# Optimization experiments

Hardware: AMD Instinct MI355X
Metric: run time of the kernel (lower is better)

## Reference

```python
import jax, jax.numpy as jnp
import numpy as np

B, NS, NF, D, H = 64, 16, 4096, 128, 256  # batch, n_slots, n_feat, slot_dim, mlp_hidden
EPS_LN = 1e-5
EPS_ATT = 1e-8


def _layernorm(x, g, b):
    mu = x.mean(-1, keepdims=True)
    var = x.var(-1, keepdims=True)
    return (x - mu) / jnp.sqrt(var + EPS_LN) * g + b


def setup_inputs() -> dict:
    key = jax.random.key(0)
    ks = jax.random.split(key, 8)
    s = 0.02  # init scale for weights
    return {
        "t": jnp.zeros((), jnp.float32),
        "slots": jax.random.normal(ks[0], (B, NS, D), jnp.float32),
        "k": jax.random.normal(ks[1], (B, NF, D), jnp.float32),
        "v": jax.random.normal(ks[2], (B, NF, D), jnp.float32),
        "Wq": jax.random.normal(ks[3], (D, D), jnp.float32) * s,           # eqx Linear weight [out,in], no bias
        "ln_slots_g": jnp.ones((D,), jnp.float32),
        "ln_slots_b": jnp.zeros((D,), jnp.float32),
        "W_ih": jax.random.normal(ks[4], (3 * D, D), jnp.float32) * s,     # GRUCell input weights
        "W_hh": jax.random.normal(ks[5], (3 * D, D), jnp.float32) * s,     # GRUCell hidden weights
        "b_ih": jnp.zeros((3 * D,), jnp.float32),
        "b_n": jnp.zeros((D,), jnp.float32),
        "ln_ff_g": jnp.ones((D,), jnp.float32),
        "ln_ff_b": jnp.zeros((D,), jnp.float32),
        "W0": jax.random.normal(ks[6], (H, D), jnp.float32) * s,
        "b0": jnp.zeros((H,), jnp.float32),
        "W1": jax.random.normal(ks[7], (D, H), jnp.float32) * s,
        "b1": jnp.zeros((D,), jnp.float32),
    }


def reference(t, slots, k, v, Wq, ln_slots_g, ln_slots_b,
              W_ih, W_hh, b_ih, b_n, ln_ff_g, ln_ff_b, W0, b0, W1, b1):
    scale = D ** (-0.5)
    # LayerNorm over slot features, then query projection
    slots_norm = _layernorm(slots, ln_slots_g, ln_slots_b)
    q = jnp.einsum('bnd,ed->bne', slots_norm, Wq)                    # [B,NS,D]
    # Doubly-normalized slot attention: softmax over slots (axis=1), renorm over features
    att_logits = jnp.einsum('bnd,bmd->bnm', q, k) * scale            # [B,NS,NF]
    att = jax.nn.softmax(att_logits, axis=1)
    att = att / (att.sum(axis=-1, keepdims=True) + EPS_ATT)
    attended = jnp.einsum('bnm,bmd->bnd', att, v)                    # [B,NS,D]
    # GRUCell (equinox semantics): gates order (reset, input, new)
    igates = jnp.einsum('bnd,ed->bne', attended, W_ih) + b_ih        # [B,NS,3D]
    hgates = jnp.einsum('bnd,ed->bne', slots, W_hh)                  # [B,NS,3D]
    ir, ii, inew = jnp.split(igates, 3, axis=-1)
    hr, hi, hnew = jnp.split(hgates, 3, axis=-1)
    reset = jax.nn.sigmoid(ir + hr)
    inp = jax.nn.sigmoid(ii + hi)
    new = jnp.tanh(inew + reset * (hnew + b_n))
    gru_out = new + inp * (slots - new)                              # [B,NS,D]
    # LayerNorm -> MLP residual
    gru_normed = _layernorm(gru_out, ln_ff_g, ln_ff_b)
    h = jax.nn.relu(jnp.einsum('bnd,hd->bnh', gru_normed, W0) + b0)
    h = jnp.einsum('bnh,dh->bnd', h, W1) + b1
    target = gru_out + h
    return target - slots
```

## Files before the change

### kernel.cpp

```cpp
#include <hip/hip_runtime.h>
#include <hip/hip_bf16.h>
#include <math.h>

#define B_  64
#define NS_ 16
#define NF_ 4096
#define D_  128
#define H_  256


typedef __attribute__((ext_vector_type(8))) short bf16x8;
typedef __attribute__((ext_vector_type(4))) float f32x4;

__device__ __forceinline__ bf16x8 as_bf16x8(uint4 u) {
    union { uint4 u; bf16x8 h; } c; c.u = u; return c.h;
}

__device__ __forceinline__ unsigned int pk_bf16(float a, float b) {
    unsigned int ua = __float_as_uint(a), ub = __float_as_uint(b);
    ua = (ua + 0x7FFFu + ((ua >> 16) & 1u)) >> 16;
    ub = (ub + 0x7FFFu + ((ub >> 16) & 1u)) >> 16;
    return ua | (ub << 16);
}

__device__ __forceinline__ float dot4(float4 a, float4 b) {
    return a.x * b.x + a.y * b.y + a.z * b.z + a.w * b.w;
}

__global__ __launch_bounds__(128) void k_q(
    const float* __restrict__ slots, const float* __restrict__ Wq,
    const float* __restrict__ lng, const float* __restrict__ lnb,
    unsigned int* __restrict__ q_out, float* __restrict__ acc, float* __restrict__ den) {
    const int b = blockIdx.x;
    const int t = threadIdx.x;
    __shared__ float sl_s[16][128];
    __shared__ float norm_s[16][128];
    __shared__ float st_s[16][8][2];
    __shared__ float mu_s[16], rs_s[16];
    __shared__ float q_s[16][128];

    const float4* sp = (const float4*)(slots + (size_t)b * 2048);
#pragma unroll
    for (int i = 0; i < 4; ++i) {
        int f = i * 128 + t;
        *(float4*)&sl_s[f >> 5][(f & 31) * 4] = sp[f];
    }
    __syncthreads();

    {
        int n = t >> 3, j = t & 7;
        float s1 = 0.f, s2 = 0.f;
#pragma unroll
        for (int d2 = 0; d2 < 16; ++d2) {
            float x = sl_s[n][j * 16 + d2];
            s1 += x; s2 += x * x;
        }
        st_s[n][j][0] = s1; st_s[n][j][1] = s2;
    }
    __syncthreads();
    if (t < 16) {
        float s1 = 0.f, s2 = 0.f;
#pragma unroll
        for (int j = 0; j < 8; ++j) { s1 += st_s[t][j][0]; s2 += st_s[t][j][1]; }
        float mu = s1 * (1.0f / 128.0f);
        float var = s2 * (1.0f / 128.0f) - mu * mu;
        mu_s[t] = mu;
        rs_s[t] = rsqrtf(var + 1e-5f);
    }
    __syncthreads();

    float gl = lng[t], bl = lnb[t];
#pragma unroll
    for (int n = 0; n < 16; ++n)
        norm_s[n][t] = (sl_s[n][t] - mu_s[n]) * rs_s[n] * gl + bl;
    __syncthreads();

    const float4* wq = (const float4*)(Wq + (size_t)t * 128);
    float qn[16];
#pragma unroll
    for (int n = 0; n < 16; ++n) qn[n] = 0.f;
#pragma unroll 4
    for (int j = 0; j < 32; ++j) {
        float4 w4 = wq[j];
#pragma unroll
        for (int n = 0; n < 16; ++n) qn[n] += dot4(w4, *(const float4*)&norm_s[n][4 * j]);
    }
#pragma unroll
    for (int n = 0; n < 16; ++n) q_s[n][t] = qn[n];

    float4 z4 = make_float4(0.f, 0.f, 0.f, 0.f);
    float4* ab = (float4*)(acc + (size_t)b * 2048);
#pragma unroll
    for (int i = 0; i < 4; ++i) ab[i * 128 + t] = z4;
    if (t < 16) den[b * 16 + t] = 0.f;
    __syncthreads();

    unsigned int* qo = q_out + (size_t)b * 1024;
#pragma unroll
    for (int i = 0; i < 8; ++i) {
        int u = i * 128 + t;
        int n = u >> 6, e2 = u & 63;
        qo[n * 64 + e2] = pk_bf16(q_s[n][2 * e2], q_s[n][2 * e2 + 1]);
    }
}

template<int PART>
__global__ __launch_bounds__(256) void k_attn(
    const float* __restrict__ kg_, const float* __restrict__ vg_,
    const unsigned int* __restrict__ q_u, float* __restrict__ acc_g,
    float* __restrict__ part, float* __restrict__ denom_g) {
    const int t = threadIdx.x;
    const int w = t >> 6, l = t & 63;
    const int b = blockIdx.y;
    const int lm = l & 15;
    const int g  = l >> 4;
    const int dcol = t & 127;
    const int nh = t >> 7;

    __shared__ unsigned int lds_u[5632];
    unsigned int* k_s = lds_u;
    float*        p_s = (float*)(lds_u + 4352);

    uint4 qA[4];
    {
        const uint4* qb = (const uint4*)q_u + ((b * 16 + lm) * 16);
#pragma unroll
        for (int kk = 0; kk < 4; ++kk) qA[kk] = qb[kk * 4 + g];
    }

    float acc[16];
#pragma unroll
    for (int i = 0; i < 16; ++i) acc[i] = 0.f;
    float dn[4] = {0.f, 0.f, 0.f, 0.f};

    const size_t mbase = (size_t)b * NF_ + blockIdx.x * 256;
    const float4* kg4 = (const float4*)kg_ + (mbase + w * 16) * 32;
    const float*  vgp = vg_ + mbase * 128 + dcol;

    for (int sub = 0; sub < 4; ++sub) {
        const float* vt = vgp + (size_t)(sub * 64 + nh * 32) * 128;

        const float4* kp = kg4 + sub * 64 * 32;
        float4 ka[4], kb4[4];
#pragma unroll
        for (int i = 0; i < 4; ++i) ka[i] = kp[i * 64 + l];
#pragma unroll
        for (int i = 0; i < 4; ++i) kb4[i] = kp[(4 + i) * 64 + l];

        float vva[8], vvb[8];
#pragma unroll
        for (int i = 0; i < 8; ++i) vva[i] = vt[i * 128];
#pragma unroll
        for (int i = 0; i < 8; ++i) vvb[i] = vt[(8 + i) * 128];

#pragma unroll
        for (int i = 0; i < 4; ++i) {
            int r = w * 16 + 2 * i + (l >> 5);
            *(uint2*)&k_s[r * 68 + 2 * (l & 31)] =
                make_uint2(pk_bf16(ka[i].x, ka[i].y), pk_bf16(ka[i].z, ka[i].w));
        }
#pragma unroll
        for (int i = 0; i < 4; ++i) {
            int r = w * 16 + 2 * (4 + i) + (l >> 5);
            *(uint2*)&k_s[r * 68 + 2 * (l & 31)] =
                make_uint2(pk_bf16(kb4[i].x, kb4[i].y), pk_bf16(kb4[i].z, kb4[i].w));
        }

        f32x4 sacc = {0.f, 0.f, 0.f, 0.f};
#pragma unroll
        for (int kk = 0; kk < 4; ++kk) {
            uint4 kf = *(const uint4*)&k_s[(w * 16 + lm) * 68 + kk * 16 + g * 4];
            sacc = __builtin_amdgcn_mfma_f32_16x16x32_bf16(
                as_bf16x8(qA[kk]), as_bf16x8(kf), sacc, 0, 0, 0);
        }
        const float scale = 0.08838834764831845f;
        float e0 = __expf(sacc[0] * scale);
        float e1 = __expf(sacc[1] * scale);
        float e2 = __expf(sacc[2] * scale);
        float e3 = __expf(sacc[3] * scale);
        float se = (e0 + e1) + (e2 + e3);
        se += __shfl_xor(se, 16);
        se += __shfl_xor(se, 32);
        float rse = __builtin_amdgcn_rcpf(se);
        float4 pv4 = make_float4(e0 * rse, e1 * rse, e2 * rse, e3 * rse);
        dn[0] += pv4.x; dn[1] += pv4.y; dn[2] += pv4.z; dn[3] += pv4.w;
        *(float4*)&p_s[(w * 16 + lm) * 20 + g * 4] = pv4;
        __syncthreads();

#define PV_CONSUME(VREG, BASE)                                              \
        {                                                                   \
            _Pragma("unroll")                                               \
            for (int i = 0; i < 8; ++i) {                                   \
                int m = nh * 32 + (BASE) + i;                               \
                float vvi = VREG[i];                                        \
                float4 pa = *(const float4*)&p_s[m * 20 + 0];               \
                float4 pb = *(const float4*)&p_s[m * 20 + 4];               \
                float4 pc = *(const float4*)&p_s[m * 20 + 8];               \
                float4 pd = *(const float4*)&p_s[m * 20 + 12];              \
                acc[0]  = fmaf(pa.x, vvi, acc[0]);                          \
                acc[1]  = fmaf(pa.y, vvi, acc[1]);                          \
                acc[2]  = fmaf(pa.z, vvi, acc[2]);                          \
                acc[3]  = fmaf(pa.w, vvi, acc[3]);                          \
                acc[4]  = fmaf(pb.x, vvi, acc[4]);                          \
                acc[5]  = fmaf(pb.y, vvi, acc[5]);                          \
                acc[6]  = fmaf(pb.z, vvi, acc[6]);                          \
                acc[7]  = fmaf(pb.w, vvi, acc[7]);                          \
                acc[8]  = fmaf(pc.x, vvi, acc[8]);                          \
                acc[9]  = fmaf(pc.y, vvi, acc[9]);                          \
                acc[10] = fmaf(pc.z, vvi, acc[10]);                         \
                acc[11] = fmaf(pc.w, vvi, acc[11]);                         \
                acc[12] = fmaf(pd.x, vvi, acc[12]);                         \
                acc[13] = fmaf(pd.y, vvi, acc[13]);                         \
                acc[14] = fmaf(pd.z, vvi, acc[14]);                         \
                acc[15] = fmaf(pd.w, vvi, acc[15]);                         \
            }                                                               \
        }
        PV_CONSUME(vva, 0)
#pragma unroll
        for (int i = 0; i < 8; ++i) vva[i] = vt[(16 + i) * 128];
        PV_CONSUME(vvb, 8)
#pragma unroll
        for (int i = 0; i < 8; ++i) vvb[i] = vt[(24 + i) * 128];
        PV_CONSUME(vva, 16)
        PV_CONSUME(vvb, 24)
#undef PV_CONSUME
        __syncthreads();
    }

#pragma unroll
    for (int m = 1; m <= 8; m <<= 1) {
#pragma unroll
        for (int r = 0; r < 4; ++r) dn[r] += __shfl_xor(dn[r], m);
    }
    if (lm == 0) {
#pragma unroll
        for (int r = 0; r < 4; ++r)
            atomicAdd(denom_g + b * 16 + g * 4 + r, dn[r]);
    }
    float* red = (float*)lds_u;
    if (nh == 1) {
#pragma unroll
        for (int n = 0; n < 16; ++n) red[dcol * 17 + n] = acc[n];
    }
    __syncthreads();
    if (nh == 0) {
        if (PART) {
            float* base = part + ((size_t)(b * 16 + blockIdx.x) * 16) * 128 + dcol;
#pragma unroll
            for (int n = 0; n < 16; ++n)
                base[n * 128] = acc[n] + red[dcol * 17 + n];
        } else {
            float* base = acc_g + (size_t)b * 2048 + dcol;
#pragma unroll
            for (int n = 0; n < 16; ++n)
                atomicAdd(base + n * 128, acc[n] + red[dcol * 17 + n]);
        }
    }
}

template<int PART>
__global__ __launch_bounds__(256) void k_final(
    const float* __restrict__ acc_g, const float* __restrict__ part,
    const float* __restrict__ denom_g, const float* __restrict__ slots,
    const float* __restrict__ W_ih, const float* __restrict__ W_hh,
    const float* __restrict__ b_ih, const float* __restrict__ b_n,
    const float* __restrict__ ffg, const float* __restrict__ ffb,
    const float* __restrict__ W0, const float* __restrict__ b0,
    const float* __restrict__ W1, const float* __restrict__ b1,
    float* __restrict__ out) {
    const int bn0 = blockIdx.x * 4;
    const int t = threadIdx.x;
    __shared__ float att_s[4][128], slot_s[4][128];
    __shared__ float gates_s[4][4][128];
    __shared__ float gru_s[4][128], gn_s[4][128];
    __shared__ float h_s[4][256];

#pragma unroll
    for (int idx = t; idx < 512; idx += 256) {
        int bi = idx >> 7, d = idx & 127;
        int bn = bn0 + bi;
        float den = denom_g[bn] + 1e-8f;
        float s;
        if (PART) {
            const float* pp = part + ((size_t)(bn >> 4) * 256 + (bn & 15)) * 128 + d;
            s = 0.f;
#pragma unroll
            for (int c = 0; c < 16; ++c) s += pp[c * 2048];
        } else {
            s = acc_g[(size_t)bn * 128 + d];
        }
        att_s[bi][d] = s / den;
        slot_s[bi][d] = slots[(size_t)bn * 128 + d];
    }
    __syncthreads();

    for (int g = t; g < 384; g += 256) {
        const float4* wi = (const float4*)(W_ih + (size_t)g * 128);
        const float4* wh = (const float4*)(W_hh + (size_t)g * 128);
        float si[4] = {0.f, 0.f, 0.f, 0.f}, sh[4] = {0.f, 0.f, 0.f, 0.f};
#pragma unroll 4
        for (int j = 0; j < 32; ++j) {
            float4 wi4 = wi[j], wh4 = wh[j];
#pragma unroll
            for (int bi = 0; bi < 4; ++bi) {
                si[bi] += dot4(wi4, *(const float4*)&att_s[bi][4 * j]);
                sh[bi] += dot4(wh4, *(const float4*)&slot_s[bi][4 * j]);
            }
        }
        float bih = b_ih[g];
        int d = g & 127;
#pragma unroll
        for (int bi = 0; bi < 4; ++bi) {
            if (g < 128)       gates_s[bi][0][d] = si[bi] + sh[bi] + bih;
            else if (g < 256)  gates_s[bi][1][d] = si[bi] + sh[bi] + bih;
            else { gates_s[bi][2][d] = si[bi] + bih; gates_s[bi][3][d] = sh[bi]; }
        }
    }
    __syncthreads();

    {
        int bi = t >> 6, l = t & 63;
        float gr[2], s1 = 0.f, s2 = 0.f;
#pragma unroll
        for (int h = 0; h < 2; ++h) {
            int d = l + 64 * h;
            float rr = 1.f / (1.f + __expf(-gates_s[bi][0][d]));
            float ii = 1.f / (1.f + __expf(-gates_s[bi][1][d]));
            float nv = tanhf(gates_s[bi][2][d] + rr * (gates_s[bi][3][d] + b_n[d]));
            float gru = nv + ii * (slot_s[bi][d] - nv);
            gr[h] = gru;
            gru_s[bi][d] = gru;
            s1 += gru; s2 += gru * gru;
        }
#pragma unroll
        for (int m = 1; m < 64; m <<= 1) { s1 += __shfl_xor(s1, m); s2 += __shfl_xor(s2, m); }
        float mu = s1 * (1.0f / 128.0f);
        float var = s2 * (1.0f / 128.0f) - mu * mu;
        float rstd = rsqrtf(var + 1e-5f);
#pragma unroll
        for (int h = 0; h < 2; ++h) {
            int d = l + 64 * h;
            gn_s[bi][d] = (gr[h] - mu) * rstd * ffg[d] + ffb[d];
        }
    }
    __syncthreads();

    {
        const float4* w0 = (const float4*)(W0 + (size_t)t * 128);
        float s[4] = {0.f, 0.f, 0.f, 0.f};
#pragma unroll 4
        for (int j = 0; j < 32; ++j) {
            float4 w4 = w0[j];
#pragma unroll
            for (int bi = 0; bi < 4; ++bi) s[bi] += dot4(w4, *(const float4*)&gn_s[bi][4 * j]);
        }
        float b0v = b0[t];
#pragma unroll
        for (int bi = 0; bi < 4; ++bi) h_s[bi][t] = fmaxf(s[bi] + b0v, 0.f);
    }
    __syncthreads();

    {
        int dr = t & 127, bp = (t >> 7) * 2;
        const float4* w1 = (const float4*)(W1 + (size_t)dr * 256);
        float s[2] = {0.f, 0.f};
#pragma unroll 4
        for (int j = 0; j < 64; ++j) {
            float4 w4 = w1[j];
#pragma unroll
            for (int u = 0; u < 2; ++u) s[u] += dot4(w4, *(const float4*)&h_s[bp + u][4 * j]);
        }
        float b1v = b1[dr];
#pragma unroll
        for (int u = 0; u < 2; ++u) {
            int bi = bp + u;
            out[(size_t)(bn0 + bi) * 128 + dr] = gru_s[bi][dr] + s[u] + b1v - slot_s[bi][dr];
        }
    }
}

extern "C" void kernel_launch(void* const* d_in, const int* in_sizes, int n_in,
                              void* d_out, int out_size, void* d_ws, size_t ws_size,
                              hipStream_t stream) {
    const float* slots = (const float*)d_in[1];
    const float* k     = (const float*)d_in[2];
    const float* v     = (const float*)d_in[3];
    const float* Wq    = (const float*)d_in[4];
    const float* lng   = (const float*)d_in[5];
    const float* lnb   = (const float*)d_in[6];
    const float* W_ih  = (const float*)d_in[7];
    const float* W_hh  = (const float*)d_in[8];
    const float* b_ih  = (const float*)d_in[9];
    const float* b_n   = (const float*)d_in[10];
    const float* ffg   = (const float*)d_in[11];
    const float* ffb   = (const float*)d_in[12];
    const float* W0    = (const float*)d_in[13];
    const float* b0    = (const float*)d_in[14];
    const float* W1    = (const float*)d_in[15];
    const float* b1    = (const float*)d_in[16];

    char* ws = (char*)d_ws;
    unsigned int* q_u = (unsigned int*)ws;
    float* acc  = (float*)(ws + 262144);
    float* den  = (float*)(ws + 786432);
    float* partp = (float*)(ws + 1048576);

    const bool use_part = (ws_size >= (size_t)1048576 + 64u * 16u * 16u * 128u * 4u);

    k_q<<<dim3(B_), dim3(128), 0, stream>>>(slots, Wq, lng, lnb, q_u, acc, den);
    if (use_part) {
        k_attn<1><<<dim3(16, B_), dim3(256), 0, stream>>>(k, v, q_u, acc, partp, den);
        k_final<1><<<dim3(256), dim3(256), 0, stream>>>(acc, partp, den, slots,
                                                        W_ih, W_hh, b_ih, b_n, ffg, ffb,
                                                        W0, b0, W1, b1, (float*)d_out);
    } else {
        k_attn<0><<<dim3(16, B_), dim3(256), 0, stream>>>(k, v, q_u, acc, partp, den);
        k_final<0><<<dim3(256), dim3(256), 0, stream>>>(acc, partp, den, slots,
                                                        W_ih, W_hh, b_ih, b_n, ffg, ffb,
                                                        W0, b0, W1, b1, (float*)d_out);
    }
}
```

Before: 368.6 us.

## Double-buffer bf16 attention probabilities in LDS and drop per-iteration barrier

After: 430.3 us. +16.7%, slower.

```diff
diff --git a/kernel.cpp b/kernel.cpp
--- a/kernel.cpp
+++ b/kernel.cpp
@@ -15,6 +15,9 @@
 __device__ __forceinline__ bf16x8 as_bf16x8(uint4 u) {
     union { uint4 u; bf16x8 h; } c; c.u = u; return c.h;
 }
+
+__device__ __forceinline__ float bflo(unsigned int u) { return __uint_as_float(u << 16); }
+__device__ __forceinline__ float bfhi(unsigned int u) { return __uint_as_float(u & 0xffff0000u); }
 
 __device__ __forceinline__ unsigned int pk_bf16(float a, float b) {
     unsigned int ua = __float_as_uint(a), ub = __float_as_uint(b);
@@ -117,9 +120,9 @@
     const int dcol = t & 127;
     const int nh = t >> 7;
 
-    __shared__ unsigned int lds_u[5632];
+    __shared__ unsigned int lds_u[5888];
     unsigned int* k_s = lds_u;
-    float*        p_s = (float*)(lds_u + 4352);
+    unsigned int* p0  = lds_u + 4352;
 
     uint4 qA[4];
     {
@@ -137,7 +140,9 @@
     const float4* kg4 = (const float4*)kg_ + (mbase + w * 16) * 32;
     const float*  vgp = vg_ + mbase * 128 + dcol;
 
+#pragma unroll 1
     for (int sub = 0; sub < 4; ++sub) {
+        unsigned int* p_s = p0 + (sub & 1) * 768;
         const float* vt = vgp + (size_t)(sub * 64 + nh * 32) * 128;
 
         const float4* kp = kg4 + sub * 64 * 32;
@@ -182,9 +187,10 @@
         se += __shfl_xor(se, 16);
         se += __shfl_xor(se, 32);
         float rse = __builtin_amdgcn_rcpf(se);
-        float4 pv4 = make_float4(e0 * rse, e1 * rse, e2 * rse, e3 * rse);
-        dn[0] += pv4.x; dn[1] += pv4.y; dn[2] += pv4.z; dn[3] += pv4.w;
-        *(float4*)&p_s[(w * 16 + lm) * 20 + g * 4] = pv4;
+        float p0v = e0 * rse, p1v = e1 * rse, p2v = e2 * rse, p3v = e3 * rse;
+        dn[0] += p0v; dn[1] += p1v; dn[2] += p2v; dn[3] += p3v;
+        *(uint2*)&p_s[(w * 16 + lm) * 12 + 2 * g] =
+            make_uint2(pk_bf16(p0v, p1v), pk_bf16(p2v, p3v));
         __syncthreads();
 
 #define PV_CONSUME(VREG, BASE)                                              \
@@ -193,26 +199,24 @@
             for (int i = 0; i < 8; ++i) {                                   \
                 int m = nh * 32 + (BASE) + i;                               \
                 float vvi = VREG[i];                                        \
-                float4 pa = *(const float4*)&p_s[m * 20 + 0];               \
-                float4 pb = *(const float4*)&p_s[m * 20 + 4];               \
-                float4 pc = *(const float4*)&p_s[m * 20 + 8];               \
-                float4 pd = *(const float4*)&p_s[m * 20 + 12];              \
-                acc[0]  = fmaf(pa.x, vvi, acc[0]);                          \
-                acc[1]  = fmaf(pa.y, vvi, acc[1]);                          \
-                acc[2]  = fmaf(pa.z, vvi, acc[2]);                          \
-                acc[3]  = fmaf(pa.w, vvi, acc[3]);                          \
-                acc[4]  = fmaf(pb.x, vvi, acc[4]);                          \
-                acc[5]  = fmaf(pb.y, vvi, acc[5]);                          \
-                acc[6]  = fmaf(pb.z, vvi, acc[6]);                          \
-                acc[7]  = fmaf(pb.w, vvi, acc[7]);                          \
-                acc[8]  = fmaf(pc.x, vvi, acc[8]);                          \
-                acc[9]  = fmaf(pc.y, vvi, acc[9]);                          \
-                acc[10] = fmaf(pc.z, vvi, acc[10]);                         \
-                acc[11] = fmaf(pc.w, vvi, acc[11]);                         \
-                acc[12] = fmaf(pd.x, vvi, acc[12]);                         \
-                acc[13] = fmaf(pd.y, vvi, acc[13]);                         \
-                acc[14] = fmaf(pd.z, vvi, acc[14]);                         \
-                acc[15] = fmaf(pd.w, vvi, acc[15]);                         \
+                uint4 pu0 = *(const uint4*)&p_s[m * 12];                    \
+                uint4 pu1 = *(const uint4*)&p_s[m * 12 + 4];                \
+                acc[0]  = fmaf(bflo(pu0.x), vvi, acc[0]);                   \
+                acc[1]  = fmaf(bfhi(pu0.x), vvi, acc[1]);                   \
+                acc[2]  = fmaf(bflo(pu0.y), vvi, acc[2]);                   \
+                acc[3]  = fmaf(bfhi(pu0.y), vvi, acc[3]);                   \
+                acc[4]  = fmaf(bflo(pu0.z), vvi, acc[4]);                   \
+                acc[5]  = fmaf(bfhi(pu0.z), vvi, acc[5]);                   \
+                acc[6]  = fmaf(bflo(pu0.w), vvi, acc[6]);                   \
+                acc[7]  = fmaf(bfhi(pu0.w), vvi, acc[7]);                   \
+                acc[8]  = fmaf(bflo(pu1.x), vvi, acc[8]);                   \
+                acc[9]  = fmaf(bfhi(pu1.x), vvi, acc[9]);                   \
+                acc[10] = fmaf(bflo(pu1.y), vvi, acc[10]);                  \
+                acc[11] = fmaf(bfhi(pu1.y), vvi, acc[11]);                  \
+                acc[12] = fmaf(bflo(pu1.z), vvi, acc[12]);                  \
+                acc[13] = fmaf(bfhi(pu1.z), vvi, acc[13]);                  \
+                acc[14] = fmaf(bflo(pu1.w), vvi, acc[14]);                  \
+                acc[15] = fmaf(bfhi(pu1.w), vvi, acc[15]);                  \
             }                                                               \
         }
         PV_CONSUME(vva, 0)
@@ -224,7 +228,6 @@
         PV_CONSUME(vva, 16)
         PV_CONSUME(vvb, 24)
 #undef PV_CONSUME
-        __syncthreads();
     }
 
 #pragma unroll
@@ -237,6 +240,7 @@
         for (int r = 0; r < 4; ++r)
             atomicAdd(denom_g + b * 16 + g * 4 + r, dn[r]);
     }
+    __syncthreads();
     float* red = (float*)lds_u;
     if (nh == 1) {
 #pragma unroll
```

## Fuse query projection into attention kernel and replace denominator atomics with partials

Applied to the files above, without the earlier changes.

Result: no change. 366.4 us (-0.6%).

```diff
diff --git a/kernel.cpp b/kernel.cpp
--- a/kernel.cpp
+++ b/kernel.cpp
@@ -27,88 +27,13 @@
     return a.x * b.x + a.y * b.y + a.z * b.z + a.w * b.w;
 }
 
-__global__ __launch_bounds__(128) void k_q(
-    const float* __restrict__ slots, const float* __restrict__ Wq,
-    const float* __restrict__ lng, const float* __restrict__ lnb,
-    unsigned int* __restrict__ q_out, float* __restrict__ acc, float* __restrict__ den) {
-    const int b = blockIdx.x;
-    const int t = threadIdx.x;
-    __shared__ float sl_s[16][128];
-    __shared__ float norm_s[16][128];
-    __shared__ float st_s[16][8][2];
-    __shared__ float mu_s[16], rs_s[16];
-    __shared__ float q_s[16][128];
-
-    const float4* sp = (const float4*)(slots + (size_t)b * 2048);
-#pragma unroll
-    for (int i = 0; i < 4; ++i) {
-        int f = i * 128 + t;
-        *(float4*)&sl_s[f >> 5][(f & 31) * 4] = sp[f];
-    }
-    __syncthreads();
-
-    {
-        int n = t >> 3, j = t & 7;
-        float s1 = 0.f, s2 = 0.f;
-#pragma unroll
-        for (int d2 = 0; d2 < 16; ++d2) {
-            float x = sl_s[n][j * 16 + d2];
-            s1 += x; s2 += x * x;
-        }
-        st_s[n][j][0] = s1; st_s[n][j][1] = s2;
-    }
-    __syncthreads();
-    if (t < 16) {
-        float s1 = 0.f, s2 = 0.f;
-#pragma unroll
-        for (int j = 0; j < 8; ++j) { s1 += st_s[t][j][0]; s2 += st_s[t][j][1]; }
-        float mu = s1 * (1.0f / 128.0f);
-        float var = s2 * (1.0f / 128.0f) - mu * mu;
-        mu_s[t] = mu;
-        rs_s[t] = rsqrtf(var + 1e-5f);
-    }
-    __syncthreads();
-
-    float gl = lng[t], bl = lnb[t];
-#pragma unroll
-    for (int n = 0; n < 16; ++n)
-        norm_s[n][t] = (sl_s[n][t] - mu_s[n]) * rs_s[n] * gl + bl;
-    __syncthreads();
-
-    const float4* wq = (const float4*)(Wq + (size_t)t * 128);
-    float qn[16];
-#pragma unroll
-    for (int n = 0; n < 16; ++n) qn[n] = 0.f;
-#pragma unroll 4
-    for (int j = 0; j < 32; ++j) {
-        float4 w4 = wq[j];
-#pragma unroll
-        for (int n = 0; n < 16; ++n) qn[n] += dot4(w4, *(const float4*)&norm_s[n][4 * j]);
-    }
-#pragma unroll
-    for (int n = 0; n < 16; ++n) q_s[n][t] = qn[n];
-
-    float4 z4 = make_float4(0.f, 0.f, 0.f, 0.f);
-    float4* ab = (float4*)(acc + (size_t)b * 2048);
-#pragma unroll
-    for (int i = 0; i < 4; ++i) ab[i * 128 + t] = z4;
-    if (t < 16) den[b * 16 + t] = 0.f;
-    __syncthreads();
-
-    unsigned int* qo = q_out + (size_t)b * 1024;
-#pragma unroll
-    for (int i = 0; i < 8; ++i) {
-        int u = i * 128 + t;
-        int n = u >> 6, e2 = u & 63;
-        qo[n * 64 + e2] = pk_bf16(q_s[n][2 * e2], q_s[n][2 * e2 + 1]);
-    }
-}
-
 template<int PART>
 __global__ __launch_bounds__(256) void k_attn(
     const float* __restrict__ kg_, const float* __restrict__ vg_,
-    const unsigned int* __restrict__ q_u, float* __restrict__ acc_g,
-    float* __restrict__ part, float* __restrict__ denom_g) {
+    const float* __restrict__ slots, const float* __restrict__ Wq,
+    const float* __restrict__ lng, const float* __restrict__ lnb,
+    float* __restrict__ acc_g, float* __restrict__ part,
+    float* __restrict__ pden, float* __restrict__ denom_g) {
     const int t = threadIdx.x;
     const int w = t >> 6, l = t & 63;
     const int b = blockIdx.y;
@@ -122,10 +47,75 @@
     float*        p_s = (float*)(lds_u + 4352);
 
     uint4 qA[4];
+
     {
-        const uint4* qb = (const uint4*)q_u + ((b * 16 + lm) * 16);
-#pragma unroll
-        for (int kk = 0; kk < 4; ++kk) qA[kk] = qb[kk * 4 + g];
+        float* sl   = (float*)lds_u;
+        float* q_s  = (float*)(lds_u + 2048);
+        float* st   = (float*)(lds_u + 4096);
+        float* mu_s = (float*)(lds_u + 4608);
+        float* rs_s = (float*)(lds_u + 4624);
+
+        const float4* sp = (const float4*)(slots + (size_t)b * 2048);
+#pragma unroll
+        for (int i = 0; i < 2; ++i) {
+            int f = i * 256 + t;
+            *(float4*)&sl[f * 4] = sp[f];
+        }
+        __syncthreads();
+        {
+            int n = t >> 4, j = t & 15;
+            float s1 = 0.f, s2 = 0.f;
+#pragma unroll
+            for (int d2 = 0; d2 < 8; ++d2) {
+                float x = sl[n * 128 + j * 8 + d2];
+                s1 += x; s2 += x * x;
+            }
+            st[(n * 16 + j) * 2 + 0] = s1;
+            st[(n * 16 + j) * 2 + 1] = s2;
+        }
+        __syncthreads();
+        if (t < 16) {
+            float s1 = 0.f, s2 = 0.f;
+#pragma unroll
+            for (int j = 0; j < 16; ++j) {
+                s1 += st[(t * 16 + j) * 2];
+                s2 += st[(t * 16 + j) * 2 + 1];
+            }
+            float mu = s1 * (1.0f / 128.0f);
+            float var = s2 * (1.0f / 128.0f) - mu * mu;
+            mu_s[t] = mu;
+            rs_s[t] = rsqrtf(var + 1e-5f);
+        }
+        __syncthreads();
+#pragma unroll
+        for (int i = 0; i < 8; ++i) {
+            int idx = i * 256 + t;
+            int n = idx >> 7, d = idx & 127;
+            sl[idx] = (sl[idx] - mu_s[n]) * rs_s[n] * lng[d] + lnb[d];
+        }
+        __syncthreads();
+        {
+            int e = t & 127, n0 = (t >> 7) * 8;
+            const float4* wq = (const float4*)(Wq + (size_t)e * 128);
+            float qn[8] = {0.f, 0.f, 0.f, 0.f, 0.f, 0.f, 0.f, 0.f};
+#pragma unroll 4
+            for (int j = 0; j < 32; ++j) {
+                float4 w4 = wq[j];
+#pragma unroll
+                for (int r = 0; r < 8; ++r)
+                    qn[r] += dot4(w4, *(const float4*)&sl[(n0 + r) * 128 + 4 * j]);
+            }
+#pragma unroll
+            for (int r = 0; r < 8; ++r) q_s[(n0 + r) * 128 + e] = qn[r];
+        }
+        __syncthreads();
+#pragma unroll
+        for (int kk = 0; kk < 4; ++kk) {
+            const float* qr = &q_s[lm * 128 + kk * 32 + g * 8];
+            qA[kk] = make_uint4(pk_bf16(qr[0], qr[1]), pk_bf16(qr[2], qr[3]),
+                                pk_bf16(qr[4], qr[5]), pk_bf16(qr[6], qr[7]));
+        }
+        __syncthreads();
     }
 
     float acc[16];
@@ -232,10 +222,10 @@
 #pragma unroll
         for (int r = 0; r < 4; ++r) dn[r] += __shfl_xor(dn[r], m);
     }
+    float* pden_s = (float*)(lds_u + 4352);
     if (lm == 0) {
 #pragma unroll
-        for (int r = 0; r < 4; ++r)
-            atomicAdd(denom_g + b * 16 + g * 4 + r, dn[r]);
+        for (int r = 0; r < 4; ++r) pden_s[w * 16 + g * 4 + r] = dn[r];
     }
     float* red = (float*)lds_u;
     if (nh == 1) {
@@ -243,6 +233,11 @@
         for (int n = 0; n < 16; ++n) red[dcol * 17 + n] = acc[n];
     }
     __syncthreads();
+    if (t < 16) {
+        float s = pden_s[t] + pden_s[16 + t] + pden_s[32 + t] + pden_s[48 + t];
+        if (PART) pden[((size_t)b * 16 + blockIdx.x) * 16 + t] = s;
+        else      atomicAdd(denom_g + b * 16 + t, s);
+    }
     if (nh == 0) {
         if (PART) {
             float* base = part + ((size_t)(b * 16 + blockIdx.x) * 16) * 128 + dcol;
@@ -261,7 +256,8 @@
 template<int PART>
 __global__ __launch_bounds__(256) void k_final(
     const float* __restrict__ acc_g, const float* __restrict__ part,
-    const float* __restrict__ denom_g, const float* __restrict__ slots,
+    const float* __restrict__ pden, const float* __restrict__ denom_g,
+    const float* __restrict__ slots,
     const float* __restrict__ W_ih, const float* __restrict__ W_hh,
     const float* __restrict__ b_ih, const float* __restrict__ b_n,
     const float* __restrict__ ffg, const float* __restrict__ ffb,
@@ -274,22 +270,37 @@
     __shared__ float gates_s[4][4][128];
     __shared__ float gru_s[4][128], gn_s[4][128];
     __shared__ float h_s[4][256];
+    __shared__ float deni_s[4];
+
+    if (t < 4) {
+        int bn = bn0 + t;
+        float s = 1e-8f;
+        if (PART) {
+            const float* pd = pden + (size_t)(bn >> 4) * 256 + (bn & 15);
+#pragma unroll
+            for (int c = 0; c < 16; ++c) s += pd[c * 16];
+        } else {
+            s += denom_g[bn];
+        }
+        deni_s[t] = 1.f / s;
+    }
+    __syncthreads();
 
 #pragma unroll
     for (int idx = t; idx < 512; idx += 256) {
         int bi = idx >> 7, d = idx & 127;
         int bn = bn0 + bi;
-        float den = denom_g[bn] + 1e-8f;
         float s;
         if (PART) {
-            const float* pp = part + ((size_t)(bn >> 4) * 256 + (bn & 15)) * 128 + d;
+            const float* pp = part +
+                ((size_t)(bn >> 4) * 256 + (size_t)(bn & 15)) * 128 + d;
             s = 0.f;
-#pragma unroll
-            for (int c = 0; c < 16; ++c) s += pp[c * 2048];
+#pragma unroll 8
+            for (int c = 0; c < 16; ++c) s += pp[(size_t)c * 2048];
         } else {
             s = acc_g[(size_t)bn * 128 + d];
         }
-        att_s[bi][d] = s / den;
+        att_s[bi][d] = s * deni_s[bi];
         slot_s[bi][d] = slots[(size_t)bn * 128 + d];
     }
     __syncthreads();
@@ -400,23 +411,25 @@
     const float* b1    = (const float*)d_in[16];
 
     char* ws = (char*)d_ws;
-    unsigned int* q_u = (unsigned int*)ws;
-    float* acc  = (float*)(ws + 262144);
-    float* den  = (float*)(ws + 786432);
+    float* acc   = (float*)(ws + 262144);
+    float* den   = (float*)(ws + 786432);
+    float* pden  = (float*)(ws + 790528);
     float* partp = (float*)(ws + 1048576);
 
     const bool use_part = (ws_size >= (size_t)1048576 + 64u * 16u * 16u * 128u * 4u);
 
-    k_q<<<dim3(B_), dim3(128), 0, stream>>>(slots, Wq, lng, lnb, q_u, acc, den);
     if (use_part) {
-        k_attn<1><<<dim3(16, B_), dim3(256), 0, stream>>>(k, v, q_u, acc, partp, den);
-        k_final<1><<<dim3(256), dim3(256), 0, stream>>>(acc, partp, den, slots,
-                                                        W_ih, W_hh, b_ih, b_n, ffg, ffb,
-                                                        W0, b0, W1, b1, (float*)d_out);
+        k_attn<1><<<dim3(16, B_), dim3(256), 0, stream>>>(
+            k, v, slots, Wq, lng, lnb, acc, partp, pden, den);
+        k_final<1><<<dim3(256), dim3(256), 0, stream>>>(
+            acc, partp, pden, den, slots, W_ih, W_hh, b_ih, b_n, ffg, ffb,
+            W0, b0, W1, b1, (float*)d_out);
     } else {
-        k_attn<0><<<dim3(16, B_), dim3(256), 0, stream>>>(k, v, q_u, acc, partp, den);
-        k_final<0><<<dim3(256), dim3(256), 0, stream>>>(acc, partp, den, slots,
-                                                        W_ih, W_hh, b_ih, b_n, ffg, ffb,
-                                                        W0, b0, W1, b1, (float*)d_out);
-    }
-}
+        hipMemsetAsync(ws + 262144, 0, 528384, stream);
+        k_attn<0><<<dim3(16, B_), dim3(256), 0, stream>>>(
+            k, v, slots, Wq, lng, lnb, acc, partp, pden, den);
+        k_final<0><<<dim3(256), dim3(256), 0, stream>>>(
+            acc, partp, pden, den, slots, W_ih, W_hh, b_ih, b_n, ffg, ffb,
+            W0, b0, W1, b1, (float*)d_out);
+    }
+}
```
